# Performance work log

Measured on AMD Instinct MI355X. Metric: run time of the kernel, lower is better.

The kernel has to match this reference:

```python
import jax, jax.numpy as jnp
import numpy as np
import math

B, S, CZ, H, CH = 1, 384, 128, 4, 32


def setup_inputs() -> dict:
    key = jax.random.key(0)
    ks = jax.random.split(key, 12)
    sd = 0.02
    return {
        "z": jax.random.normal(ks[0], (B, S, S, CZ), dtype=jnp.float32),
        "ln_w": jnp.ones((CZ,), dtype=jnp.float32),
        "ln_b": jnp.zeros((CZ,), dtype=jnp.float32),
        "Wq": jax.random.normal(ks[1], (H * CH, CZ), dtype=jnp.float32) * sd,
        "Wk": jax.random.normal(ks[2], (CH, CZ), dtype=jnp.float32) * sd,
        "Wv": jax.random.normal(ks[3], (CH, CZ), dtype=jnp.float32) * sd,
        "Wb": jax.random.normal(ks[4], (H, CZ), dtype=jnp.float32) * sd,
        "Wg": jax.random.normal(ks[5], (H * CH, CZ), dtype=jnp.float32) * sd,
        "bg": jnp.zeros((H * CH,), dtype=jnp.float32),
        "Wo": jax.random.normal(ks[6], (CZ, H * CH), dtype=jnp.float32) * sd,
        "bo": jnp.zeros((CZ,), dtype=jnp.float32),
    }


def reference(z, ln_w, ln_b, Wq, Wk, Wv, Wb, Wg, bg, Wo, bo):
    b_, s_, _, cz = z.shape
    h = Wb.shape[0]          # n_heads
    ch = Wk.shape[0]         # c_hidden
    # LayerNorm over c_z (eps = 1e-5, torch default)
    mu = jnp.mean(z, axis=-1, keepdims=True)
    var = jnp.mean(jnp.square(z - mu), axis=-1, keepdims=True)
    zn = (z - mu) * jax.lax.rsqrt(var + 1e-5) * ln_w + ln_b
    # projections (starting=True: attend along rows i over key index k)
    q = (zn @ Wq.T).reshape(b_, s_, s_, h, ch)   # [B,I,J,H,C]
    k = zn @ Wk.T                                 # [B,I,K,C] shared across heads
    v = zn @ Wv.T                                 # [B,I,K,C]
    bias = zn @ Wb.T                              # [B,I,J,H]
    g = jax.nn.sigmoid(zn @ Wg.T + bg)            # [B,I,J,H*C]
    scale = 1.0 / math.sqrt(ch)
    logits = jnp.einsum('bijhc,bikc->bihjk', q, k) * scale  # [B,I,H,J,K]
    # NOTE: faithful to source — bias broadcasts along the KEY axis (softmax-invariant)
    logits = logits + jnp.transpose(bias, (0, 1, 3, 2))[..., None]
    w = jax.nn.softmax(logits, axis=-1)           # [B,I,H,J,K]
    o = jnp.einsum('bihjk,bikc->bijhc', w, v).reshape(b_, s_, s_, h * ch)
    o = g * o
    return o @ Wo.T + bo
```

## Files before the change

kernel.cpp:

```cpp
#include <hip/hip_runtime.h>
#include <math.h>


typedef unsigned short u16;
typedef __attribute__((ext_vector_type(8))) short short8;
typedef __attribute__((ext_vector_type(4))) float float4v;

union U8 { short8 s; u16 h[8]; };

__device__ __forceinline__ float bf2f(u16 x){
    unsigned v = ((unsigned)x) << 16;
    float f; __builtin_memcpy(&f, &v, 4);
    return f;
}
__device__ __forceinline__ u16 f2bf(float f){
    unsigned v; __builtin_memcpy(&v, &f, 4);
    unsigned r = (v + 0x7FFFu + ((v >> 16) & 1u)) >> 16;
    return (u16)r;
}
__device__ __forceinline__ short8 pack8f(const float* p){
    const float4 a = ((const float4*)p)[0];
    const float4 b = ((const float4*)p)[1];
    U8 u;
    u.h[0]=f2bf(a.x); u.h[1]=f2bf(a.y); u.h[2]=f2bf(a.z); u.h[3]=f2bf(a.w);
    u.h[4]=f2bf(b.x); u.h[5]=f2bf(b.y); u.h[6]=f2bf(b.z); u.h[7]=f2bf(b.w);
    return u.s;
}

__global__ __launch_bounds__(256) void k1_ln_proj(
    const float* __restrict__ z, const float* __restrict__ lnw, const float* __restrict__ lnb,
    const float* __restrict__ Wq, const float* __restrict__ Wk, const float* __restrict__ Wv,
    const float* __restrict__ Wg, const float* __restrict__ bg,
    u16* __restrict__ Qbuf, u16* __restrict__ KVbuf, u16* __restrict__ Gbuf)
{
    __shared__ __align__(16) u16 zn[64][136];
    const int tid = threadIdx.x;
    const long rowg0 = (long)blockIdx.x * 64;

    {
        const int r = tid >> 2, p = tid & 3;
        const float* src = z + (rowg0 + r) * 128 + p * 32;
        float x[32];
        #pragma unroll
        for (int q = 0; q < 8; q++){
            const float4 v = ((const float4*)src)[q];
            x[q*4+0]=v.x; x[q*4+1]=v.y; x[q*4+2]=v.z; x[q*4+3]=v.w;
        }
        float s = 0.f, ss = 0.f;
        #pragma unroll
        for (int t = 0; t < 32; t++){ s += x[t]; ss += x[t]*x[t]; }
        s += __shfl_xor(s, 1);  ss += __shfl_xor(ss, 1);
        s += __shfl_xor(s, 2);  ss += __shfl_xor(ss, 2);
        const float mean = s * (1.f/128.f);
        const float var  = ss * (1.f/128.f) - mean*mean;
        const float rstd = rsqrtf(var + 1e-5f);
        #pragma unroll
        for (int t = 0; t < 32; t++){
            const int c = p*32 + t;
            zn[r][c] = f2bf((x[t]-mean)*rstd*lnw[c] + lnb[c]);
        }
    }
    __syncthreads();

    const int lane = tid & 63, wave = tid >> 6;
    const int l15 = lane & 15, quad = lane >> 4;

    short8 A[4][4];
    #pragma unroll
    for (int m = 0; m < 4; m++)
        #pragma unroll
        for (int ks = 0; ks < 4; ks++)
            A[m][ks] = *(const short8*)&zn[m*16 + l15][ks*32 + quad*8];

    #pragma unroll
    for (int g = 0; g < 5; g++){
        const int nt = wave*5 + g;
        const float* Wp; int nbase, kind;
        if (nt < 8)       { Wp = Wq; nbase = nt*16;      kind = 0; }
        else if (nt < 10) { Wp = Wk; nbase = (nt-8)*16;  kind = 1; }
        else if (nt < 12) { Wp = Wv; nbase = (nt-10)*16; kind = 2; }
        else              { Wp = Wg; nbase = (nt-12)*16; kind = 3; }
        const float* bp = Wp + (nbase + l15)*128 + quad*8;
        short8 B[4];
        #pragma unroll
        for (int ks = 0; ks < 4; ks++) B[ks] = pack8f(bp + ks*32);
        #pragma unroll
        for (int m = 0; m < 4; m++){
            float4v c = {0.f,0.f,0.f,0.f};
            #pragma unroll
            for (int ks = 0; ks < 4; ks++)
                c = __builtin_amdgcn_mfma_f32_16x16x32_bf16(A[m][ks], B[ks], c, 0, 0, 0);
            const int n = nt*16 + l15;
            #pragma unroll
            for (int r = 0; r < 4; r++){
                const long row = rowg0 + m*16 + quad*4 + r;
                const float v = c[r];
                if (kind == 0)      Qbuf[row*128 + n] = f2bf(v * 0.17677669529663689f);
                else if (kind == 1) KVbuf[row*64 + (n - 128)] = f2bf(v);
                else if (kind == 2) KVbuf[row*64 + (n - 160) + 32] = f2bf(v);
                else {
                    const float gg = 1.f/(1.f + __expf(-(v + bg[n - 192])));
                    Gbuf[row*128 + (n - 192)] = f2bf(gg);
                }
            }
        }
    }
}

__global__ __launch_bounds__(256, 2) void k2_attn(
    const u16* __restrict__ KVbuf, const u16* __restrict__ Gbuf, u16* __restrict__ QObuf)
{
    __shared__ __align__(16) u16 Ks[384][40];
    __shared__ __align__(16) u16 Vt[32][392];
    __shared__ __align__(16) u16 Pb[4][16][200];
    const int i = blockIdx.x >> 2, h = blockIdx.x & 3;
    const int tid = threadIdx.x;
    {
        const u16* kvsrc = KVbuf + (long)i * 384 * 64;
        for (int idx = tid; idx < 384*8; idx += 256){
            const int k = idx >> 3, c8 = idx & 7;
            U8 d; d.s = *(const short8*)(kvsrc + k*64 + c8*8);
            if (c8 < 4) *(short8*)&Ks[k][c8*8] = d.s;
            else {
                const int c0 = (c8 - 4) * 8;
                #pragma unroll
                for (int jj = 0; jj < 8; jj++) Vt[c0 + jj][k] = d.h[jj];
            }
        }
    }
    __syncthreads();

    const int lane = tid & 63, wave = tid >> 6;
    const int l15 = lane & 15, quad = lane >> 4;
    const u16* qbase = QObuf + (long)i * 384 * 128 + h * 32;
    const u16* gbase = Gbuf  + (long)i * 384 * 128 + h * 32;
    u16* obase = QObuf + (long)i * 384 * 128 + h * 32;

    for (int t = 0; t < 6; t++){
        const int j0 = (wave*6 + t) * 16;
        const short8 aq = *(const short8*)(qbase + (long)(j0 + l15)*128 + quad*8);
        float4v acc[24];
        #pragma unroll
        for (int kt = 0; kt < 24; kt++){
            const short8 bk = *(const short8*)&Ks[kt*16 + l15][quad*8];
            float4v zero = {0.f,0.f,0.f,0.f};
            acc[kt] = __builtin_amdgcn_mfma_f32_16x16x32_bf16(aq, bk, zero, 0, 0, 0);
        }
        float inv[4];
        #pragma unroll
        for (int r = 0; r < 4; r++){
            float mx = -1e30f;
            #pragma unroll
            for (int kt = 0; kt < 24; kt++) mx = fmaxf(mx, acc[kt][r]);
            mx = fmaxf(mx, __shfl_xor(mx, 1));
            mx = fmaxf(mx, __shfl_xor(mx, 2));
            mx = fmaxf(mx, __shfl_xor(mx, 4));
            mx = fmaxf(mx, __shfl_xor(mx, 8));
            float sum = 0.f;
            #pragma unroll
            for (int kt = 0; kt < 24; kt++){ acc[kt][r] = __expf(acc[kt][r] - mx); sum += acc[kt][r]; }
            sum += __shfl_xor(sum, 1);
            sum += __shfl_xor(sum, 2);
            sum += __shfl_xor(sum, 4);
            sum += __shfl_xor(sum, 8);
            inv[r] = 1.f / sum;
        }
        float4v oacc[2] = {{0.f,0.f,0.f,0.f},{0.f,0.f,0.f,0.f}};
        #pragma unroll
        for (int kt = 0; kt < 12; kt++)
            #pragma unroll
            for (int r = 0; r < 4; r++)
                Pb[wave][quad*4 + r][kt*16 + l15] = f2bf(acc[kt][r]);
        #pragma unroll
        for (int kk = 0; kk < 6; kk++){
            const short8 ap = *(const short8*)&Pb[wave][l15][kk*32 + quad*8];
            #pragma unroll
            for (int ct = 0; ct < 2; ct++){
                const short8 bv = *(const short8*)&Vt[ct*16 + l15][kk*32 + quad*8];
                oacc[ct] = __builtin_amdgcn_mfma_f32_16x16x32_bf16(ap, bv, oacc[ct], 0, 0, 0);
            }
        }
        #pragma unroll
        for (int kt = 12; kt < 24; kt++)
            #pragma unroll
            for (int r = 0; r < 4; r++)
                Pb[wave][quad*4 + r][(kt-12)*16 + l15] = f2bf(acc[kt][r]);
        #pragma unroll
        for (int kk = 6; kk < 12; kk++){
            const short8 ap = *(const short8*)&Pb[wave][l15][(kk-6)*32 + quad*8];
            #pragma unroll
            for (int ct = 0; ct < 2; ct++){
                const short8 bv = *(const short8*)&Vt[ct*16 + l15][kk*32 + quad*8];
                oacc[ct] = __builtin_amdgcn_mfma_f32_16x16x32_bf16(ap, bv, oacc[ct], 0, 0, 0);
            }
        }
        #pragma unroll
        for (int ct = 0; ct < 2; ct++){
            const int c = ct*16 + l15;
            #pragma unroll
            for (int r = 0; r < 4; r++){
                const int row = j0 + quad*4 + r;
                const float gv = bf2f(gbase[(long)row*128 + c]);
                obase[(long)row*128 + c] = f2bf(gv * (oacc[ct][r] * inv[r]));
            }
        }
    }
}

__global__ __launch_bounds__(256) void k3_outproj(
    const u16* __restrict__ Obuf, const float* __restrict__ Wo, const float* __restrict__ bo,
    float* __restrict__ out)
{
    const int tid = threadIdx.x, lane = tid & 63, wave = tid >> 6;
    const int l15 = lane & 15, quad = lane >> 4;
    const long row0 = (long)blockIdx.x * 64;
    short8 B[2][4];
    #pragma unroll
    for (int g = 0; g < 2; g++){
        const float* bp = Wo + ((wave*2 + g)*16 + l15)*128 + quad*8;
        #pragma unroll
        for (int ks = 0; ks < 4; ks++) B[g][ks] = pack8f(bp + ks*32);
    }
    #pragma unroll
    for (int m = 0; m < 4; m++){
        short8 A[4];
        const u16* ap = Obuf + (row0 + m*16 + l15)*128 + quad*8;
        #pragma unroll
        for (int ks = 0; ks < 4; ks++) A[ks] = *(const short8*)(ap + ks*32);
        #pragma unroll
        for (int g = 0; g < 2; g++){
            float4v c = {0.f,0.f,0.f,0.f};
            #pragma unroll
            for (int ks = 0; ks < 4; ks++)
                c = __builtin_amdgcn_mfma_f32_16x16x32_bf16(A[ks], B[g][ks], c, 0, 0, 0);
            const int n = (wave*2 + g)*16 + l15;
            const float bov = bo[n];
            #pragma unroll
            for (int r = 0; r < 4; r++){
                const long row = row0 + m*16 + quad*4 + r;
                out[row*128 + n] = c[r] + bov;
            }
        }
    }
}

extern "C" void kernel_launch(void* const* d_in, const int* in_sizes, int n_in,
                              void* d_out, int out_size, void* d_ws, size_t ws_size,
                              hipStream_t stream)
{
    (void)in_sizes; (void)n_in; (void)out_size; (void)ws_size;
    const float* z   = (const float*)d_in[0];
    const float* lnw = (const float*)d_in[1];
    const float* lnb = (const float*)d_in[2];
    const float* Wq  = (const float*)d_in[3];
    const float* Wk  = (const float*)d_in[4];
    const float* Wv  = (const float*)d_in[5];
    const float* Wg  = (const float*)d_in[7];
    const float* bg  = (const float*)d_in[8];
    const float* Wo  = (const float*)d_in[9];
    const float* bo  = (const float*)d_in[10];

    u16* Qbuf = (u16*)d_ws;
    u16* KV   = Qbuf + 147456L*128;
    u16* Gbuf = (u16*)d_out;

    k1_ln_proj<<<dim3(2304), dim3(256), 0, stream>>>(z, lnw, lnb, Wq, Wk, Wv, Wg, bg,
                                                     Qbuf, KV, Gbuf);
    k2_attn<<<dim3(1536), dim3(256), 0, stream>>>(KV, Gbuf, Qbuf);
    k3_outproj<<<dim3(2304), dim3(256), 0, stream>>>(Qbuf, Wo, bo, (float*)d_out);
}
```

Baseline: 402.1 us.

## Pre-convert weights to bf16 once and swap MFMA operands for vectorized stores

Adds small kernels that convert the projection weights (with the Q scale folded in) and Wo to bf16 once per call, so each block of the projection and output kernels loads bf16 fragments instead of converting fp32 weights itself. The MFMA operand order is swapped so each lane holds four consecutive output columns, which turns scalar 2-byte and 4-byte stores into 8-byte and 16-byte vector stores. The cost is two extra launches and scratch buffers placed in the output and KV regions, which depends on those regions being free at the moment they are used.

```diff
diff --git a/kernel.cpp b/kernel.cpp
--- a/kernel.cpp
+++ b/kernel.cpp
@@ -4,9 +4,11 @@
 
 typedef unsigned short u16;
 typedef __attribute__((ext_vector_type(8))) short short8;
+typedef __attribute__((ext_vector_type(4))) short short4v;
 typedef __attribute__((ext_vector_type(4))) float float4v;
 
 union U8 { short8 s; u16 h[8]; };
+union U4 { short4v s; u16 h[4]; };
 
 __device__ __forceinline__ float bf2f(u16 x){
     unsigned v = ((unsigned)x) << 16;
@@ -18,19 +20,41 @@
     unsigned r = (v + 0x7FFFu + ((v >> 16) & 1u)) >> 16;
     return (u16)r;
 }
-__device__ __forceinline__ short8 pack8f(const float* p){
+__device__ __forceinline__ short8 pack8f_s(const float* p, float s){
     const float4 a = ((const float4*)p)[0];
     const float4 b = ((const float4*)p)[1];
     U8 u;
-    u.h[0]=f2bf(a.x); u.h[1]=f2bf(a.y); u.h[2]=f2bf(a.z); u.h[3]=f2bf(a.w);
-    u.h[4]=f2bf(b.x); u.h[5]=f2bf(b.y); u.h[6]=f2bf(b.z); u.h[7]=f2bf(b.w);
+    u.h[0]=f2bf(a.x*s); u.h[1]=f2bf(a.y*s); u.h[2]=f2bf(a.z*s); u.h[3]=f2bf(a.w*s);
+    u.h[4]=f2bf(b.x*s); u.h[5]=f2bf(b.y*s); u.h[6]=f2bf(b.z*s); u.h[7]=f2bf(b.w*s);
     return u.s;
+}
+
+__global__ __launch_bounds__(256) void k0a_wconv(
+    const float* __restrict__ Wq, const float* __restrict__ Wk,
+    const float* __restrict__ Wv, const float* __restrict__ Wg,
+    u16* __restrict__ Wbf)
+{
+    const int i = blockIdx.x * 256 + threadIdx.x;
+    const int e = i * 8;
+    const int n = e >> 7, c0 = e & 127;
+    const float* src; float s = 1.f;
+    if (n < 128)      { src = Wq + n*128 + c0; s = 0.17677669529663689f; }
+    else if (n < 160) { src = Wk + (n-128)*128 + c0; }
+    else if (n < 192) { src = Wv + (n-160)*128 + c0; }
+    else              { src = Wg + (n-192)*128 + c0; }
+    *(short8*)(Wbf + e) = pack8f_s(src, s);
+}
+
+__global__ __launch_bounds__(256) void k0b_wconv(
+    const float* __restrict__ Wo, u16* __restrict__ WoBf)
+{
+    const int e = (blockIdx.x * 256 + threadIdx.x) * 8;
+    *(short8*)(WoBf + e) = pack8f_s(Wo + e, 1.f);
 }
 
 __global__ __launch_bounds__(256) void k1_ln_proj(
     const float* __restrict__ z, const float* __restrict__ lnw, const float* __restrict__ lnb,
-    const float* __restrict__ Wq, const float* __restrict__ Wk, const float* __restrict__ Wv,
-    const float* __restrict__ Wg, const float* __restrict__ bg,
+    const u16* __restrict__ Wbf, const float* __restrict__ bg,
     u16* __restrict__ Qbuf, u16* __restrict__ KVbuf, u16* __restrict__ Gbuf)
 {
     __shared__ __align__(16) u16 zn[64][136];
@@ -65,43 +89,51 @@
     const int lane = tid & 63, wave = tid >> 6;
     const int l15 = lane & 15, quad = lane >> 4;
 
-    short8 A[4][4];
+    short8 ZN[4][4];
     #pragma unroll
     for (int m = 0; m < 4; m++)
         #pragma unroll
         for (int ks = 0; ks < 4; ks++)
-            A[m][ks] = *(const short8*)&zn[m*16 + l15][ks*32 + quad*8];
+            ZN[m][ks] = *(const short8*)&zn[m*16 + l15][ks*32 + quad*8];
 
     #pragma unroll
     for (int g = 0; g < 5; g++){
         const int nt = wave*5 + g;
-        const float* Wp; int nbase, kind;
-        if (nt < 8)       { Wp = Wq; nbase = nt*16;      kind = 0; }
-        else if (nt < 10) { Wp = Wk; nbase = (nt-8)*16;  kind = 1; }
-        else if (nt < 12) { Wp = Wv; nbase = (nt-10)*16; kind = 2; }
-        else              { Wp = Wg; nbase = (nt-12)*16; kind = 3; }
-        const float* bp = Wp + (nbase + l15)*128 + quad*8;
-        short8 B[4];
-        #pragma unroll
-        for (int ks = 0; ks < 4; ks++) B[ks] = pack8f(bp + ks*32);
+        const u16* wp = Wbf + (nt*16 + l15)*128 + quad*8;
+        short8 WF[4];
+        #pragma unroll
+        for (int ks = 0; ks < 4; ks++) WF[ks] = *(const short8*)(wp + ks*32);
+        const int n0 = nt*16 + quad*4;
         #pragma unroll
         for (int m = 0; m < 4; m++){
             float4v c = {0.f,0.f,0.f,0.f};
             #pragma unroll
             for (int ks = 0; ks < 4; ks++)
-                c = __builtin_amdgcn_mfma_f32_16x16x32_bf16(A[m][ks], B[ks], c, 0, 0, 0);
-            const int n = nt*16 + l15;
-            #pragma unroll
-            for (int r = 0; r < 4; r++){
-                const long row = rowg0 + m*16 + quad*4 + r;
-                const float v = c[r];
-                if (kind == 0)      Qbuf[row*128 + n] = f2bf(v * 0.17677669529663689f);
-                else if (kind == 1) KVbuf[row*64 + (n - 128)] = f2bf(v);
-                else if (kind == 2) KVbuf[row*64 + (n - 160) + 32] = f2bf(v);
-                else {
-                    const float gg = 1.f/(1.f + __expf(-(v + bg[n - 192])));
-                    Gbuf[row*128 + (n - 192)] = f2bf(gg);
-                }
+                c = __builtin_amdgcn_mfma_f32_16x16x32_bf16(WF[ks], ZN[m][ks], c, 0, 0, 0);
+            const long row = rowg0 + m*16 + l15;
+            if (nt < 8){
+                U4 u;
+                #pragma unroll
+                for (int r = 0; r < 4; r++) u.h[r] = f2bf(c[r]);
+                *(short4v*)(Qbuf + row*128 + n0) = u.s;
+            } else if (nt < 10){
+                U4 u;
+                #pragma unroll
+                for (int r = 0; r < 4; r++) u.h[r] = f2bf(c[r]);
+                *(short4v*)(KVbuf + row*64 + (n0 - 128)) = u.s;
+            } else if (nt < 12){
+                U4 u;
+                #pragma unroll
+                for (int r = 0; r < 4; r++) u.h[r] = f2bf(c[r]);
+                *(short4v*)(KVbuf + row*64 + (n0 - 160) + 32) = u.s;
+            } else {
+                const float4 b4 = *(const float4*)&bg[n0 - 192];
+                U4 u;
+                u.h[0] = f2bf(1.f/(1.f + __expf(-(c[0] + b4.x))));
+                u.h[1] = f2bf(1.f/(1.f + __expf(-(c[1] + b4.y))));
+                u.h[2] = f2bf(1.f/(1.f + __expf(-(c[2] + b4.z))));
+                u.h[3] = f2bf(1.f/(1.f + __expf(-(c[3] + b4.w))));
+                *(short4v*)(Gbuf + row*128 + (n0 - 192)) = u.s;
             }
         }
     }
@@ -208,38 +240,38 @@
 }
 
 __global__ __launch_bounds__(256) void k3_outproj(
-    const u16* __restrict__ Obuf, const float* __restrict__ Wo, const float* __restrict__ bo,
+    const u16* __restrict__ Obuf, const u16* __restrict__ WoBf, const float* __restrict__ bo,
     float* __restrict__ out)
 {
     const int tid = threadIdx.x, lane = tid & 63, wave = tid >> 6;
     const int l15 = lane & 15, quad = lane >> 4;
     const long row0 = (long)blockIdx.x * 64;
-    short8 B[2][4];
+    short8 WF[2][4];
     #pragma unroll
     for (int g = 0; g < 2; g++){
-        const float* bp = Wo + ((wave*2 + g)*16 + l15)*128 + quad*8;
-        #pragma unroll
-        for (int ks = 0; ks < 4; ks++) B[g][ks] = pack8f(bp + ks*32);
+        const u16* wp = WoBf + ((wave*2 + g)*16 + l15)*128 + quad*8;
+        #pragma unroll
+        for (int ks = 0; ks < 4; ks++) WF[g][ks] = *(const short8*)(wp + ks*32);
     }
     #pragma unroll
     for (int m = 0; m < 4; m++){
-        short8 A[4];
+        short8 OF[4];
         const u16* ap = Obuf + (row0 + m*16 + l15)*128 + quad*8;
         #pragma unroll
-        for (int ks = 0; ks < 4; ks++) A[ks] = *(const short8*)(ap + ks*32);
+        for (int ks = 0; ks < 4; ks++) OF[ks] = *(const short8*)(ap + ks*32);
         #pragma unroll
         for (int g = 0; g < 2; g++){
             float4v c = {0.f,0.f,0.f,0.f};
             #pragma unroll
             for (int ks = 0; ks < 4; ks++)
-                c = __builtin_amdgcn_mfma_f32_16x16x32_bf16(A[ks], B[g][ks], c, 0, 0, 0);
-            const int n = (wave*2 + g)*16 + l15;
-            const float bov = bo[n];
-            #pragma unroll
-            for (int r = 0; r < 4; r++){
-                const long row = row0 + m*16 + quad*4 + r;
-                out[row*128 + n] = c[r] + bov;
-            }
+                c = __builtin_amdgcn_mfma_f32_16x16x32_bf16(WF[g][ks], OF[ks], c, 0, 0, 0);
+            const int n0 = (wave*2 + g)*16 + quad*4;
+            const float4 b4 = *(const float4*)&bo[n0];
+            const long row = row0 + m*16 + l15;
+            float4 o4;
+            o4.x = c[0] + b4.x; o4.y = c[1] + b4.y;
+            o4.z = c[2] + b4.z; o4.w = c[3] + b4.w;
+            *(float4*)(out + row*128 + n0) = o4;
         }
     }
 }
@@ -263,9 +295,13 @@
     u16* Qbuf = (u16*)d_ws;
     u16* KV   = Qbuf + 147456L*128;
     u16* Gbuf = (u16*)d_out;
-
-    k1_ln_proj<<<dim3(2304), dim3(256), 0, stream>>>(z, lnw, lnb, Wq, Wk, Wv, Wg, bg,
+    u16* Wbf  = Gbuf + 147456L*128;
+    u16* WoBf = KV;
+
+    k0a_wconv<<<dim3(20), dim3(256), 0, stream>>>(Wq, Wk, Wv, Wg, Wbf);
+    k1_ln_proj<<<dim3(2304), dim3(256), 0, stream>>>(z, lnw, lnb, Wbf, bg,
                                                      Qbuf, KV, Gbuf);
     k2_attn<<<dim3(1536), dim3(256), 0, stream>>>(KV, Gbuf, Qbuf);
-    k3_outproj<<<dim3(2304), dim3(256), 0, stream>>>(Qbuf, Wo, bo, (float*)d_out);
-}
+    k0b_wconv<<<dim3(8), dim3(256), 0, stream>>>(Wo, WoBf);
+    k3_outproj<<<dim3(2304), dim3(256), 0, stream>>>(Qbuf, WoBf, bo, (float*)d_out);
+}
```

After: 335.9 us. -16.5%, faster.
